# Performance work log

Hardware: AMD Instinct MI355X
Metric: run time of the kernel (lower is better)

## Reference

```python
import jax, jax.numpy as jnp
import numpy as np

NEG = -1e20

def _rope(x):
    # x: (N, L, H, D). Original buffers use inv_freq over D with D/2 entries;
    # sin/cos tiled to full D to broadcast (original code's einsum was under-specified for 4D).
    L, D = x.shape[1], x.shape[3]
    inv_freq = 1.0 / (10000.0 ** (jnp.arange(0, D, 2, dtype=jnp.float32) / D))
    t = jnp.arange(L, dtype=jnp.float32)
    freqs = t[:, None] * inv_freq[None, :]            # (L, D/2)
    sin = jnp.concatenate([jnp.sin(freqs)] * 2, -1)[None, :, None, :]  # (1,L,1,D)
    cos = jnp.concatenate([jnp.cos(freqs)] * 2, -1)[None, :, None, :]
    return x * cos + jnp.flip(x, -1) * sin

def setup_inputs() -> dict:
    key = jax.random.key(0)
    ks = jax.random.split(key, 8)
    N, L, E, H = 2, 1024, 2048, 16
    D = E // H
    s = 0.02
    return {
        "values": jax.random.normal(ks[0], (N, L, E), jnp.float32),
        "keys": jax.random.normal(ks[1], (N, L, E), jnp.float32),
        "queries": jax.random.normal(ks[2], (N, L, E), jnp.float32),
        "mask": jax.random.randint(ks[3], (N, 1, L, L), 0, 2, jnp.int32),
        "Wv": jax.random.normal(ks[4], (D, D), jnp.float32) * s,
        "Wk": jax.random.normal(ks[5], (D, D), jnp.float32) * s,
        "Wq": jax.random.normal(ks[6], (D, D), jnp.float32) * s,
        "Wo": jax.random.normal(ks[7], (E, E), jnp.float32) * s,
        "bo": jnp.zeros((E,), jnp.float32),
    }

def reference(values, keys, queries, mask, Wv, Wk, Wq, Wo, bo):
    N, L, E = queries.shape
    H = 16
    D = E // H
    v = values.reshape(N, L, H, D)
    k = keys.reshape(N, L, H, D)
    q = queries.reshape(N, L, H, D)
    q = _rope(q)
    k = _rope(k)
    # per-head linears (nn.Linear: x @ W.T)
    v = jnp.einsum('nlhd,od->nlho', v, Wv)
    k = jnp.einsum('nlhd,od->nlho', k, Wk)
    q = jnp.einsum('nlhd,od->nlho', q, Wq)
    energy = jnp.einsum('nqhd,nkhd->nhqk', q, k)
    energy = jnp.where(mask == 0, NEG, energy)
    attn = jax.nn.softmax(energy / jnp.sqrt(jnp.float32(E)), axis=3)
    out = jnp.einsum('nhqk,nkhd->nqhd', attn, v).reshape(N, L, E)
    return out @ Wo.T + bo
```

## Files before the change

kernel.cpp:

```cpp
#include <hip/hip_runtime.h>

#define LQ 1024
#define EMB 2048
#define NH 16
#define HD 128
#define RSCALE 0.022097086912079608f

typedef unsigned short u16x8 __attribute__((ext_vector_type(8)));
typedef __bf16 bf16x8 __attribute__((ext_vector_type(8)));
typedef float f32x4 __attribute__((ext_vector_type(4)));
typedef short s16x4 __attribute__((ext_vector_type(4)));

typedef const __attribute__((address_space(1))) unsigned int* gas_t;
typedef __attribute__((address_space(3))) unsigned int* las_t;

__device__ __forceinline__ void glds16(const void* g, void* l){
  __builtin_amdgcn_global_load_lds((gas_t)g, (las_t)l, 16, 0, 0);
}
__device__ __forceinline__ unsigned short f2b(float f){
  unsigned int x = __float_as_uint(f);
  return (unsigned short)((x + 0x7fffu + ((x >> 16) & 1u)) >> 16);
}
__device__ __forceinline__ short f2bs(float f){
  union { __bf16 h; short s; } c; c.h = (__bf16)f; return c.s;
}
__device__ __forceinline__ bf16x8 as_bf(u16x8 u){
  union { u16x8 u; bf16x8 b; } c; c.u = u; return c.b;
}
__device__ __forceinline__ f32x4 mfma16(s16x4 a, s16x4 b, f32x4 c){
  return __builtin_amdgcn_mfma_f32_16x16x16bf16_1k(a, b, c, 0, 0, 0);
}

__global__ __launch_bounds__(256) void k_prep(const float* __restrict__ Wo,
                                              unsigned short* __restrict__ Wob,
                                              const int* __restrict__ M,
                                              unsigned long long* __restrict__ Mb){
  int bx = blockIdx.x, t = threadIdx.x;
  if (bx < 4096) {
    int i = (bx * 256 + t) * 4;
    float4 f = *(const float4*)&Wo[i];
    ushort4 u;
    u.x = f2b(f.x); u.y = f2b(f.y); u.z = f2b(f.z); u.w = f2b(f.w);
    *(ushort4*)&Wob[i] = u;
  } else {
    int w_idx = (bx - 4096) * 4 + (t >> 6);
    int lane = t & 63;
    int n = w_idx >> 14, row = (w_idx >> 4) & 1023, wc = w_idx & 15;
    int v = M[(size_t)n * (LQ * LQ) + (size_t)row * LQ + wc * 64 + lane];
    unsigned long long b = __ballot(v != 0);
    if (lane == 0) Mb[w_idx] = b;
  }
}

__global__ __launch_bounds__(256) void k_proj(
    const float* __restrict__ vals, const float* __restrict__ keys,
    const float* __restrict__ qrys,
    const float* __restrict__ Wv, const float* __restrict__ Wk,
    const float* __restrict__ Wq,
    unsigned short* __restrict__ vp, unsigned short* __restrict__ kp,
    unsigned short* __restrict__ qp)
{
  __shared__ unsigned short Xs[64 * 136];
  __shared__ unsigned short Ws[128 * 136];
  __shared__ float scC[4 * 128], scS[4 * 128];
  int t = threadIdx.x;
  int which = blockIdx.y;
  const float* X; const float* W; unsigned short* OUT; bool rope;
  if (which == 0)      { X = vals; W = Wv; OUT = vp; rope = false; }
  else if (which == 1) { X = keys; W = Wk; OUT = kp; rope = true;  }
  else                 { X = qrys; W = Wq; OUT = qp; rope = true;  }
  float qs = (which == 2) ? RSCALE : 1.0f;
  int m0 = blockIdx.x * 64;

  #pragma unroll
  for (int i = 0; i < 8; ++i) {
    int ci = t + 256 * i;
    int row = ci >> 4, ch = ci & 15;
    float4 a = *(const float4*)&W[row * 128 + ch * 8];
    float4 b = *(const float4*)&W[row * 128 + ch * 8 + 4];
    u16x8 u;
    u[0]=f2b(a.x); u[1]=f2b(a.y); u[2]=f2b(a.z); u[3]=f2b(a.w);
    u[4]=f2b(b.x); u[5]=f2b(b.y); u[6]=f2b(b.z); u[7]=f2b(b.w);
    *(u16x8*)&Ws[row * 136 + ch * 8] = u;
  }
  if (rope) {
    int l0 = (blockIdx.x * 4) & 1023;
    #pragma unroll
    for (int i = 0; i < 2; ++i) {
      int idx = t + 256 * i;
      int li = idx >> 7, d = idx & 127, j = d & 63;
      float inv = 1.0f / powf(10000.0f, (float)(2 * j) * 0.0078125f);
      float ang = (float)(l0 + li) * inv;
      scC[idx] = cosf(ang);
      scS[idx] = sinf(ang);
    }
  }
  __syncthreads();
  #pragma unroll
  for (int i = 0; i < 8; ++i) {
    int fi = t + 256 * i;
    int row = fi >> 5, dq = (fi & 31) * 4;
    int gr = m0 + row;
    float4 x = *(const float4*)&X[(size_t)gr * HD + dq];
    ushort4 u;
    if (rope) {
      int li = row >> 4;
      float4 xm = *(const float4*)&X[(size_t)gr * HD + (124 - dq)];
      float4 c  = *(const float4*)&scC[li * 128 + dq];
      float4 s  = *(const float4*)&scS[li * 128 + dq];
      u.x = f2b(x.x * c.x + xm.w * s.x);
      u.y = f2b(x.y * c.y + xm.z * s.y);
      u.z = f2b(x.z * c.z + xm.y * s.z);
      u.w = f2b(x.w * c.w + xm.x * s.w);
    } else {
      u.x = f2b(x.x); u.y = f2b(x.y); u.z = f2b(x.z); u.w = f2b(x.w);
    }
    *(ushort4*)&Xs[row * 136 + dq] = u;
  }
  __syncthreads();

  int w = t >> 6, lane = t & 63, quad = lane >> 4, n16 = lane & 15;
  f32x4 of[4][2];
  #pragma unroll
  for (int a = 0; a < 4; ++a)
    { of[a][0] = (f32x4){0.f,0.f,0.f,0.f}; of[a][1] = (f32x4){0.f,0.f,0.f,0.f}; }

  #pragma unroll
  for (int kd = 0; kd < 4; ++kd) {
    bf16x8 bfr[2];
    #pragma unroll
    for (int b2 = 0; b2 < 2; ++b2)
      bfr[b2] = as_bf(*(const u16x8*)&Ws[(w * 32 + b2 * 16 + n16) * 136 + kd * 32 + quad * 8]);
    #pragma unroll
    for (int a = 0; a < 4; ++a) {
      bf16x8 af = as_bf(*(const u16x8*)&Xs[(a * 16 + n16) * 136 + kd * 32 + quad * 8]);
      of[a][0] = __builtin_amdgcn_mfma_f32_16x16x32_bf16(af, bfr[0], of[a][0], 0, 0, 0);
      of[a][1] = __builtin_amdgcn_mfma_f32_16x16x32_bf16(af, bfr[1], of[a][1], 0, 0, 0);
    }
  }

  #pragma unroll
  for (int a = 0; a < 4; ++a) {
    #pragma unroll
    for (int b2 = 0; b2 < 2; ++b2) {
      #pragma unroll
      for (int r = 0; r < 4; ++r) {
        int m = m0 + a * 16 + quad * 4 + r;
        int n = m >> 14, l = (m >> 4) & 1023, h = m & 15;
        int o = w * 32 + b2 * 16 + n16;
        OUT[(((size_t)(n * NH + h)) * LQ + l) * HD + o] = f2b(of[a][b2][r] * qs);
      }
    }
  }
}

__global__ __launch_bounds__(256) void k_vtrans(const unsigned short* __restrict__ vp,
                                                unsigned short* __restrict__ vt){
  __shared__ unsigned short Ls[64 * 136];
  int t = threadIdx.x;
  int l0 = blockIdx.x * 64;
  size_t base = (size_t)blockIdx.y * LQ * HD;
  #pragma unroll
  for (int i = 0; i < 4; ++i) {
    int ci = t + 256 * i;
    int row = ci >> 4, ch = ci & 15;
    *(u16x8*)&Ls[row * 136 + ch * 8] =
        *(const u16x8*)&vp[base + (size_t)(l0 + row) * HD + ch * 8];
  }
  __syncthreads();
  #pragma unroll
  for (int i = 0; i < 4; ++i) {
    int idx = t + 256 * i;
    int d = idx & 127, lc = idx >> 7;
    u16x8 pk;
    #pragma unroll
    for (int j = 0; j < 8; ++j) pk[j] = Ls[(lc * 8 + j) * 136 + d];
    *(u16x8*)&vt[base + (size_t)d * LQ + l0 + lc * 8] = pk;
  }
}

__global__ __launch_bounds__(256) void k_attn(
    const unsigned short* __restrict__ qp, const unsigned short* __restrict__ kp,
    const unsigned short* __restrict__ vt, const unsigned long long* __restrict__ Mb,
    unsigned short* __restrict__ ao)
{
  __shared__ unsigned short Ks[2][64 * 128];
  __shared__ unsigned short Vt[2][128 * 64];
  __shared__ float ls[4][16];
  int t = threadIdx.x, w = t >> 6, lane = t & 63, quad = lane >> 4, n16 = lane & 15;
  int lin = blockIdx.y * gridDim.x + blockIdx.x;
  int xcd = lin & 7, j = lin >> 3;
  int bh = xcd + 8 * (j >> 4);
  int q0 = (j & 15) * 64;
  int nIdx = bh >> 4, h = bh & 15;
  size_t base = (size_t)bh * LQ * HD;
  const unsigned short* Q = qp + base;
  const unsigned short* K = kp + base;
  const unsigned short* V = vt + base;

  bf16x8 qf[4];
  #pragma unroll
  for (int kd = 0; kd < 4; ++kd)
    qf[kd] = as_bf(*(const u16x8*)&Q[(size_t)(q0 + w * 16 + n16) * HD + kd * 32 + quad * 8]);

  const unsigned long long* MbRow =
      Mb + ((size_t)nIdx * LQ + q0 + w * 16 + n16) * 16;

  f32x4 of[8];
  #pragma unroll
  for (int c = 0; c < 8; ++c) of[c] = (f32x4){0.f, 0.f, 0.f, 0.f};
  float lp = 0.f;
  int ub = (t & 192);

  #pragma unroll
  for (int i = 0; i < 4; ++i) {
    int ci = t + 256 * i;
    int krow = ci >> 4, kch = (ci & 15) ^ (krow & 7);
    glds16(&K[(size_t)krow * HD + kch * 8], &Ks[0][(ub + 256 * i) * 8]);
    int vrow = ci >> 3, vch = (ci & 7) ^ (vrow & 7);
    glds16(&V[(size_t)vrow * LQ + vch * 8], &Vt[0][(ub + 256 * i) * 8]);
  }

  for (int kt = 0; kt < 16; ++kt) {
    int cur = kt & 1;
    unsigned long long mq = MbRow[kt];
    __syncthreads();
    if (kt < 15) {
      int k1 = (kt + 1) * 64;
      #pragma unroll
      for (int i = 0; i < 4; ++i) {
        int ci = t + 256 * i;
        int krow = ci >> 4, kch = (ci & 15) ^ (krow & 7);
        glds16(&K[(size_t)(k1 + krow) * HD + kch * 8], &Ks[cur ^ 1][(ub + 256 * i) * 8]);
        int vrow = ci >> 3, vch = (ci & 7) ^ (vrow & 7);
        glds16(&V[(size_t)vrow * LQ + k1 + vch * 8], &Vt[cur ^ 1][(ub + 256 * i) * 8]);
      }
    }
    unsigned long long msh = mq >> (quad * 4);

    f32x4 sf[4];
    #pragma unroll
    for (int c = 0; c < 4; ++c) sf[c] = (f32x4){0.f, 0.f, 0.f, 0.f};
    __builtin_amdgcn_s_setprio(1);
    #pragma unroll
    for (int kd = 0; kd < 4; ++kd) {
      #pragma unroll
      for (int c = 0; c < 4; ++c) {
        int slot = (kd * 4 + quad) ^ (n16 & 7);
        bf16x8 kv = as_bf(*(const u16x8*)&Ks[cur][(c * 16 + n16) * 128 + slot * 8]);
        sf[c] = __builtin_amdgcn_mfma_f32_16x16x32_bf16(kv, qf[kd], sf[c], 0, 0, 0);
      }
    }
    __builtin_amdgcn_s_setprio(0);
    #pragma unroll
    for (int c = 0; c < 4; ++c) {
      s16x4 pa;
      #pragma unroll
      for (int r = 0; r < 4; ++r) {
        int bit = (int)((msh >> (c * 16 + r)) & 1ull);
        float p = bit ? __expf(sf[c][r]) : 0.f;
        lp += p;
        pa[r] = f2bs(p);
      }
      int cc = 2 * c + (quad >> 1);
      __builtin_amdgcn_s_setprio(1);
      #pragma unroll
      for (int c2 = 0; c2 < 8; ++c2) {
        int row = c2 * 16 + n16;
        int slot = cc ^ (n16 & 7);
        s16x4 vv = *(const s16x4*)&Vt[cur][row * 64 + slot * 8 + (quad & 1) * 4];
        of[c2] = mfma16(pa, vv, of[c2]);
      }
      __builtin_amdgcn_s_setprio(0);
    }
  }

  {
    float s = lp;
    s += __shfl_xor(s, 16);
    s += __shfl_xor(s, 32);
    ls[w][n16] = s;
  }
  __syncthreads();
  float linv[4];
  #pragma unroll
  for (int r = 0; r < 4; ++r) linv[r] = 1.0f / fmaxf(ls[w][quad * 4 + r], 1e-30f);

  #pragma unroll
  for (int c2 = 0; c2 < 8; ++c2) {
    #pragma unroll
    for (int r = 0; r < 4; ++r) {
      ao[((size_t)(nIdx * LQ + q0 + w * 16 + quad * 4 + r)) * EMB + h * HD + c2 * 16 + n16] =
          f2b(of[c2][r] * linv[r]);
    }
  }
}

__global__ __launch_bounds__(256) void k_outproj(
    const unsigned short* __restrict__ ao, const unsigned short* __restrict__ Wob,
    const float* __restrict__ bo, float* __restrict__ out)
{
  __shared__ unsigned short As[2][128 * 64];
  __shared__ unsigned short Bs[2][64 * 64];
  int t = threadIdx.x;
  int w = t >> 6, lane = t & 63, quad = lane >> 4, n16 = lane & 15;
  int wm = w >> 1, wo = w & 1;
  int m0 = blockIdx.x * 128, o0 = blockIdx.y * 64;
  int ub = (t & 192);

  f32x4 of[4][2];
  #pragma unroll
  for (int a = 0; a < 4; ++a)
    { of[a][0] = (f32x4){0.f,0.f,0.f,0.f}; of[a][1] = (f32x4){0.f,0.f,0.f,0.f}; }

  #pragma unroll
  for (int i = 0; i < 4; ++i) {
    int ci = t + 256 * i;
    int row = ci >> 3, ch = (ci & 7) ^ (row & 7);
    glds16(&ao[(size_t)(m0 + row) * EMB + ch * 8], &As[0][(ub + 256 * i) * 8]);
  }
  #pragma unroll
  for (int i = 0; i < 2; ++i) {
    int ci = t + 256 * i;
    int row = ci >> 3, ch = (ci & 7) ^ (row & 7);
    glds16(&Wob[(size_t)(o0 + row) * EMB + ch * 8], &Bs[0][(ub + 256 * i) * 8]);
  }

  for (int kt = 0; kt < 32; ++kt) {
    int cur = kt & 1;
    __syncthreads();
    if (kt < 31) {
      int k1 = (kt + 1) * 64;
      #pragma unroll
      for (int i = 0; i < 4; ++i) {
        int ci = t + 256 * i;
        int row = ci >> 3, ch = (ci & 7) ^ (row & 7);
        glds16(&ao[(size_t)(m0 + row) * EMB + k1 + ch * 8], &As[1 - cur][(ub + 256 * i) * 8]);
      }
      #pragma unroll
      for (int i = 0; i < 2; ++i) {
        int ci = t + 256 * i;
        int row = ci >> 3, ch = (ci & 7) ^ (row & 7);
        glds16(&Wob[(size_t)(o0 + row) * EMB + k1 + ch * 8], &Bs[1 - cur][(ub + 256 * i) * 8]);
      }
    }
    #pragma unroll
    for (int kd = 0; kd < 2; ++kd) {
      int slot0 = (kd * 4 + quad);
      bf16x8 af[4], bf[2];
      #pragma unroll
      for (int a = 0; a < 4; ++a)
        af[a] = as_bf(*(const u16x8*)&As[cur][(wm * 64 + a * 16 + n16) * 64 + (slot0 ^ (n16 & 7)) * 8]);
      #pragma unroll
      for (int b = 0; b < 2; ++b)
        bf[b] = as_bf(*(const u16x8*)&Bs[cur][(wo * 32 + b * 16 + n16) * 64 + (slot0 ^ (n16 & 7)) * 8]);
      #pragma unroll
      for (int a = 0; a < 4; ++a)
        #pragma unroll
        for (int b = 0; b < 2; ++b)
          of[a][b] = __builtin_amdgcn_mfma_f32_16x16x32_bf16(af[a], bf[b], of[a][b], 0, 0, 0);
    }
  }

  float bb[2] = { bo[o0 + wo * 32 + n16], bo[o0 + wo * 32 + 16 + n16] };
  #pragma unroll
  for (int a = 0; a < 4; ++a) {
    #pragma unroll
    for (int b = 0; b < 2; ++b) {
      #pragma unroll
      for (int r = 0; r < 4; ++r) {
        out[(size_t)(m0 + wm * 64 + a * 16 + quad * 4 + r) * EMB
            + o0 + wo * 32 + b * 16 + n16] = of[a][b][r] + bb[b];
      }
    }
  }
}

extern "C" void kernel_launch(void* const* d_in, const int* in_sizes, int n_in,
                              void* d_out, int out_size, void* d_ws, size_t ws_size,
                              hipStream_t stream) {
  (void)in_sizes; (void)n_in; (void)out_size; (void)ws_size;
  const float* vals = (const float*)d_in[0];
  const float* keys = (const float*)d_in[1];
  const float* qrys = (const float*)d_in[2];
  const int*   mask = (const int*)d_in[3];
  const float* Wv   = (const float*)d_in[4];
  const float* Wk   = (const float*)d_in[5];
  const float* Wq   = (const float*)d_in[6];
  const float* Wo   = (const float*)d_in[7];
  const float* bo   = (const float*)d_in[8];
  float* out = (float*)d_out;

  unsigned short* U  = (unsigned short*)d_ws;
  unsigned short* qp = U;
  unsigned short* kp = U + 4194304;
  unsigned short* vp = U + 8388608;
  unsigned short* vt = U + 12582912;
  unsigned short* ao = U + 16777216;
  unsigned short* Wob= U + 20971520;
  unsigned long long* Mb = (unsigned long long*)(U + 25165824);

  k_prep    <<<dim3(12288),  dim3(256), 0, stream>>>(Wo, Wob, mask, Mb);
  k_proj    <<<dim3(512, 3), dim3(256), 0, stream>>>(vals, keys, qrys, Wv, Wk, Wq,
                                                     vp, kp, qp);
  k_vtrans  <<<dim3(16, 32), dim3(256), 0, stream>>>(vp, vt);
  k_attn    <<<dim3(16, 32), dim3(256), 0, stream>>>(qp, kp, vt, Mb, ao);
  k_outproj <<<dim3(16, 32), dim3(256), 0, stream>>>(ao, Wob, bo, out);
}
```

Baseline: 214.5 us.

## Split attention key range across two wave groups in 512-thread blocks

The attention kernel now runs 8 waves per block. Two groups of four waves each handle half of every 128-key chunk over the same 64 queries, and their partial outputs and row sums are combined through shared memory at the end. This raises parallelism inside each block and halves the serial key loop per wave. In exchange it drops the load/compute double-buffer overlap, since it now loads, syncs, then computes each chunk. It also adds a reduction step and higher register and LDS pressure per block.

```diff
diff --git a/kernel.cpp b/kernel.cpp
--- a/kernel.cpp
+++ b/kernel.cpp
@@ -179,15 +179,17 @@
   }
 }
 
-__global__ __launch_bounds__(256) void k_attn(
+__global__ __launch_bounds__(512) void k_attn(
     const unsigned short* __restrict__ qp, const unsigned short* __restrict__ kp,
     const unsigned short* __restrict__ vt, const unsigned long long* __restrict__ Mb,
     unsigned short* __restrict__ ao)
 {
   __shared__ unsigned short Ks[2][64 * 128];
   __shared__ unsigned short Vt[2][128 * 64];
-  __shared__ float ls[4][16];
+  __shared__ float ls[8][16];
   int t = threadIdx.x, w = t >> 6, lane = t & 63, quad = lane >> 4, n16 = lane & 15;
+  int grp = w >> 2, wq = w & 3;
+  int ub = t & 448;
   int lin = blockIdx.y * gridDim.x + blockIdx.x;
   int xcd = lin & 7, j = lin >> 3;
   int bh = xcd + 8 * (j >> 4);
@@ -201,41 +203,35 @@
   bf16x8 qf[4];
   #pragma unroll
   for (int kd = 0; kd < 4; ++kd)
-    qf[kd] = as_bf(*(const u16x8*)&Q[(size_t)(q0 + w * 16 + n16) * HD + kd * 32 + quad * 8]);
+    qf[kd] = as_bf(*(const u16x8*)&Q[(size_t)(q0 + wq * 16 + n16) * HD + kd * 32 + quad * 8]);
 
   const unsigned long long* MbRow =
-      Mb + ((size_t)nIdx * LQ + q0 + w * 16 + n16) * 16;
+      Mb + ((size_t)nIdx * LQ + q0 + wq * 16 + n16) * 16;
 
   f32x4 of[8];
   #pragma unroll
   for (int c = 0; c < 8; ++c) of[c] = (f32x4){0.f, 0.f, 0.f, 0.f};
   float lp = 0.f;
-  int ub = (t & 192);
-
-  #pragma unroll
-  for (int i = 0; i < 4; ++i) {
-    int ci = t + 256 * i;
-    int krow = ci >> 4, kch = (ci & 15) ^ (krow & 7);
-    glds16(&K[(size_t)krow * HD + kch * 8], &Ks[0][(ub + 256 * i) * 8]);
-    int vrow = ci >> 3, vch = (ci & 7) ^ (vrow & 7);
-    glds16(&V[(size_t)vrow * LQ + vch * 8], &Vt[0][(ub + 256 * i) * 8]);
-  }
-
-  for (int kt = 0; kt < 16; ++kt) {
-    int cur = kt & 1;
-    unsigned long long mq = MbRow[kt];
+
+  for (int p = 0; p < 8; ++p) {
+    int k0 = p * 128;
     __syncthreads();
-    if (kt < 15) {
-      int k1 = (kt + 1) * 64;
-      #pragma unroll
-      for (int i = 0; i < 4; ++i) {
-        int ci = t + 256 * i;
+    #pragma unroll
+    for (int jj = 0; jj < 2; ++jj) {
+      #pragma unroll
+      for (int i = 0; i < 2; ++i) {
+        int ci = t + 512 * i;
         int krow = ci >> 4, kch = (ci & 15) ^ (krow & 7);
-        glds16(&K[(size_t)(k1 + krow) * HD + kch * 8], &Ks[cur ^ 1][(ub + 256 * i) * 8]);
+        glds16(&K[(size_t)(k0 + jj * 64 + krow) * HD + kch * 8],
+               &Ks[jj][(ub + 512 * i) * 8]);
         int vrow = ci >> 3, vch = (ci & 7) ^ (vrow & 7);
-        glds16(&V[(size_t)vrow * LQ + k1 + vch * 8], &Vt[cur ^ 1][(ub + 256 * i) * 8]);
-      }
-    }
+        glds16(&V[(size_t)vrow * LQ + k0 + jj * 64 + vch * 8],
+               &Vt[jj][(ub + 512 * i) * 8]);
+      }
+    }
+    unsigned long long mq = MbRow[2 * p + grp];
+    __syncthreads();
+
     unsigned long long msh = mq >> (quad * 4);
 
     f32x4 sf[4];
@@ -247,7 +243,7 @@
       #pragma unroll
       for (int c = 0; c < 4; ++c) {
         int slot = (kd * 4 + quad) ^ (n16 & 7);
-        bf16x8 kv = as_bf(*(const u16x8*)&Ks[cur][(c * 16 + n16) * 128 + slot * 8]);
+        bf16x8 kv = as_bf(*(const u16x8*)&Ks[grp][(c * 16 + n16) * 128 + slot * 8]);
         sf[c] = __builtin_amdgcn_mfma_f32_16x16x32_bf16(kv, qf[kd], sf[c], 0, 0, 0);
       }
     }
@@ -268,30 +264,44 @@
       for (int c2 = 0; c2 < 8; ++c2) {
         int row = c2 * 16 + n16;
         int slot = cc ^ (n16 & 7);
-        s16x4 vv = *(const s16x4*)&Vt[cur][row * 64 + slot * 8 + (quad & 1) * 4];
+        s16x4 vv = *(const s16x4*)&Vt[grp][row * 64 + slot * 8 + (quad & 1) * 4];
         of[c2] = mfma16(pa, vv, of[c2]);
       }
       __builtin_amdgcn_s_setprio(0);
     }
   }
 
+  __syncthreads();
   {
     float s = lp;
     s += __shfl_xor(s, 16);
     s += __shfl_xor(s, 32);
     ls[w][n16] = s;
   }
+  float* OF = (float*)&Ks[0][0];
+  if (grp == 1) {
+    #pragma unroll
+    for (int c2 = 0; c2 < 8; ++c2) {
+      #pragma unroll
+      for (int r = 0; r < 4; ++r) {
+        OF[(wq * 16 + quad * 4 + r) * 128 + c2 * 16 + n16] = of[c2][r];
+      }
+    }
+  }
   __syncthreads();
-  float linv[4];
-  #pragma unroll
-  for (int r = 0; r < 4; ++r) linv[r] = 1.0f / fmaxf(ls[w][quad * 4 + r], 1e-30f);
-
-  #pragma unroll
-  for (int c2 = 0; c2 < 8; ++c2) {
-    #pragma unroll
-    for (int r = 0; r < 4; ++r) {
-      ao[((size_t)(nIdx * LQ + q0 + w * 16 + quad * 4 + r)) * EMB + h * HD + c2 * 16 + n16] =
-          f2b(of[c2][r] * linv[r]);
+  if (grp == 0) {
+    float linv[4];
+    #pragma unroll
+    for (int r = 0; r < 4; ++r)
+      linv[r] = 1.0f / fmaxf(ls[wq][quad * 4 + r] + ls[wq + 4][quad * 4 + r], 1e-30f);
+    #pragma unroll
+    for (int c2 = 0; c2 < 8; ++c2) {
+      #pragma unroll
+      for (int r = 0; r < 4; ++r) {
+        float v = of[c2][r] + OF[(wq * 16 + quad * 4 + r) * 128 + c2 * 16 + n16];
+        ao[((size_t)(nIdx * LQ + q0 + wq * 16 + quad * 4 + r)) * EMB + h * HD + c2 * 16 + n16] =
+            f2b(v * linv[r]);
+      }
     }
   }
 }
@@ -404,6 +414,6 @@
   k_proj    <<<dim3(512, 3), dim3(256), 0, stream>>>(vals, keys, qrys, Wv, Wk, Wq,
                                                      vp, kp, qp);
   k_vtrans  <<<dim3(16, 32), dim3(256), 0, stream>>>(vp, vt);
-  k_attn    <<<dim3(16, 32), dim3(256), 0, stream>>>(qp, kp, vt, Mb, ao);
+  k_attn    <<<dim3(16, 32), dim3(512), 0, stream>>>(qp, kp, vt, Mb, ao);
   k_outproj <<<dim3(16, 32), dim3(256), 0, stream>>>(ao, Wob, bo, out);
 }
```

New measurement: 207.3 us. 1.03x faster.
